# Performance work log

Measured on AMD Instinct MI355X. Metric: run time of the kernel, lower is better.

The kernel has to match this reference:

```python
import jax, jax.numpy as jnp
import numpy as np

# static multi-scale feature pyramid (strides 8/16/32/64 of ~800px input)
SPATIAL = ((100, 100), (50, 50), (25, 25), (13, 13))
L = 4          # num_levels
NH = 8         # num_heads
NP = 4         # num_points
E = 256        # embed_dim
HD = E // NH   # head dim = 32
NLAYERS = 6
FFN_DIM = 1024
T = sum(h * w for h, w in SPATIAL)  # 13294 total tokens
B = 2


def _layer_norm(x, g, b, eps=1e-5):
    m = jnp.mean(x, -1, keepdims=True)
    v = jnp.mean((x - m) ** 2, -1, keepdims=True)
    return (x - m) * jax.lax.rsqrt(v + eps) * g + b


def _get_reference_points(valid_ratios):
    # valid_ratios: [B, L, 2] (wx, hy)
    refs = []
    for lvl, (H_, W_) in enumerate(SPATIAL):
        ry, rx = jnp.meshgrid(
            jnp.linspace(0.5, H_ - 0.5, H_, dtype=jnp.float32),
            jnp.linspace(0.5, W_ - 0.5, W_, dtype=jnp.float32),
            indexing='ij')
        ry = ry.reshape(-1)[None] / (valid_ratios[:, None, lvl, 1] * H_)
        rx = rx.reshape(-1)[None] / (valid_ratios[:, None, lvl, 0] * W_)
        refs.append(jnp.stack([rx, ry], -1))            # [B, H*W, 2]
    ref = jnp.concatenate(refs, 1)                       # [B, T, 2]
    return ref[:, :, None] * valid_ratios[:, None]       # [B, T, L, 2]


def _msda(value, loc, attn_w):
    # value: [B, T, NH, HD]; loc: [B, Q, NH, L, NP, 2] in [0,1]; attn_w: [B, Q, NH, L, NP]
    Bv, Tv, H, D = value.shape
    Q = loc.shape[1]
    out = jnp.zeros((Bv, Q, H, D), value.dtype)
    start = 0
    for lvl, (h, w) in enumerate(SPATIAL):
        v = value[:, start:start + h * w].transpose(0, 2, 1, 3)  # [B, NH, hw, D]
        start += h * w
        g = loc[:, :, :, lvl]                                    # [B, Q, NH, NP, 2]
        # grid_sample semantics, align_corners=False: pixel = g*size - 0.5
        x = g[..., 0] * w - 0.5
        y = g[..., 1] * h - 0.5
        x0 = jnp.floor(x).astype(jnp.int32)
        y0 = jnp.floor(y).astype(jnp.int32)
        wx = x - x0
        wy = y - y0

        def corner(ix, iy, cw):
            valid = (ix >= 0) & (ix < w) & (iy >= 0) & (iy < h)
            idx = jnp.clip(iy, 0, h - 1) * w + jnp.clip(ix, 0, w - 1)  # [B,Q,NH,NP]
            idx_t = idx.transpose(0, 2, 1, 3).reshape(Bv, H, Q * NP)
            gath = jnp.take_along_axis(v, idx_t[..., None], axis=2)    # [B,NH,QP,D]
            gath = gath.reshape(Bv, H, Q, NP, D)
            m = valid.transpose(0, 2, 1, 3)[..., None].astype(value.dtype)
            cw_t = cw.transpose(0, 2, 1, 3)[..., None]
            return gath * m * cw_t

        samp = (corner(x0, y0, (1 - wx) * (1 - wy))
                + corner(x0 + 1, y0, wx * (1 - wy))
                + corner(x0, y0 + 1, (1 - wx) * wy)
                + corner(x0 + 1, y0 + 1, wx * wy))  # [B,NH,Q,NP,D]
        out = out + jnp.einsum('bhqpd,bqhp->bqhd', samp, attn_w[:, :, :, lvl])
    return out.reshape(Bv, Q, H * D)


# offset normalizer (W, H) per level, as in Deformable-DETR
_OFF_NORM = jnp.array([[w, h] for (h, w) in SPATIAL], jnp.float32)  # [L, 2]


def _block(src, pos, ref, mask, p):
    (Wv, bv, Woff, boff, Wattn, battn, Wout, bout,
     n1g, n1b, n2g, n2b, W1, b1, W2, b2) = p
    x = _layer_norm(src, n1g, n1b)
    q = x + pos
    value = x @ Wv + bv
    value = jnp.where(mask[:, :, None], 0.0, value).reshape(B, T, NH, HD)
    off = (q @ Woff + boff).reshape(B, T, NH, L, NP, 2)
    attn = (q @ Wattn + battn).reshape(B, T, NH, L * NP)
    attn = jax.nn.softmax(attn, -1).reshape(B, T, NH, L, NP)
    loc = ref[:, :, None, :, None, :] + off / _OFF_NORM[None, None, None, :, None, :]
    attn_out = _msda(value, loc, attn) @ Wout + bout
    src = src + attn_out
    x = _layer_norm(src, n2g, n2b)
    ffn = jax.nn.relu(x @ W1 + b1) @ W2 + b2
    return src + ffn


def setup_inputs() -> dict:
    key = jax.random.key(0)
    ks = jax.random.split(key, 24)

    def rn(k, shape, scale=0.02):
        return jax.random.normal(k, shape, jnp.float32) * scale

    inp = {
        'src': jax.random.normal(ks[0], (B, T, E), jnp.float32),
        'pos': jax.random.normal(ks[1], (B, T, E), jnp.float32),
        'valid_ratios': jnp.ones((B, L, 2), jnp.float32),
        'spatial_shapes': jnp.array(SPATIAL, jnp.int32),
        'level_start_index': jnp.array(
            np.concatenate([[0], np.cumsum([h * w for h, w in SPATIAL])[:-1]]), jnp.int32),
        'mask': jnp.zeros((B, T), bool),
        # per-layer stacked parameters [NLAYERS, ...]
        'Wv': rn(ks[2], (NLAYERS, E, E)),
        'bv': jnp.zeros((NLAYERS, E), jnp.float32),
        'Woff': rn(ks[3], (NLAYERS, E, NH * L * NP * 2)),
        'boff': rn(ks[4], (NLAYERS, NH * L * NP * 2), 0.5),
        'Wattn': rn(ks[5], (NLAYERS, E, NH * L * NP)),
        'battn': jnp.zeros((NLAYERS, NH * L * NP), jnp.float32),
        'Wout': rn(ks[6], (NLAYERS, E, E)),
        'bout': jnp.zeros((NLAYERS, E), jnp.float32),
        'n1g': jnp.ones((NLAYERS, E), jnp.float32),
        'n1b': jnp.zeros((NLAYERS, E), jnp.float32),
        'n2g': jnp.ones((NLAYERS, E), jnp.float32),
        'n2b': jnp.zeros((NLAYERS, E), jnp.float32),
        'W1': rn(ks[7], (NLAYERS, E, FFN_DIM)),
        'b1': jnp.zeros((NLAYERS, FFN_DIM), jnp.float32),
        'W2': rn(ks[8], (NLAYERS, FFN_DIM, E)),
        'b2': jnp.zeros((NLAYERS, E), jnp.float32),
    }
    return inp


def reference(src, pos, valid_ratios, spatial_shapes, level_start_index, mask,
              Wv, bv, Woff, boff, Wattn, battn, Wout, bout,
              n1g, n1b, n2g, n2b, W1, b1, W2, b2):
    # spatial_shapes / level_start_index are encoded statically in SPATIAL (values match)
    ref = _get_reference_points(valid_ratios)  # [B, T, L, 2]
    x = src
    stacked = (Wv, bv, Woff, boff, Wattn, battn, Wout, bout,
               n1g, n1b, n2g, n2b, W1, b1, W2, b2)
    for i in range(NLAYERS):
        p = tuple(a[i] for a in stacked)
        x = _block(x, pos, ref, mask, p)
    return x
```

## Files before the change

kernel.cpp:

```cpp
#include <hip/hip_runtime.h>
#include <hip/hip_bf16.h>

#define NLAYERS 6
#define Bc 2
#define Tc 13294
#define Ec 256
#define NHc 8
#define FFNc 1024

#define EPI_BIAS 0
#define EPI_MASK 1
#define EPI_RES  2
#define EPI_RELU 3
#define EPI_VALOA 4

typedef __attribute__((ext_vector_type(8))) short bf16x8;
typedef __attribute__((ext_vector_type(4))) float f32x4;

typedef __attribute__((address_space(3))) unsigned int u32_lds;
typedef __attribute__((address_space(1))) unsigned int u32_glb;

__device__ __forceinline__ void gld16(const void* g, void* l) {
    __builtin_amdgcn_global_load_lds((const u32_glb*)g, (u32_lds*)l, 16, 0, 0);
}

__device__ __forceinline__ short f2bf(float f) {
    union { float f; unsigned u; } v; v.f = f;
    unsigned r = v.u + 0x7FFFu + ((v.u >> 16) & 1u);
    return (short)(r >> 16);
}
__device__ __forceinline__ float bf2f(short s) {
    union { unsigned u; float f; } v; v.u = ((unsigned)(unsigned short)s) << 16;
    return v.f;
}
__device__ __forceinline__ float bf_lo(unsigned u) {
    union { unsigned u; float f; } v; v.u = u << 16; return v.f;
}

__global__ __launch_bounds__(256) void f2bf_kernel(
    const float* __restrict__ in, short* __restrict__ out, int n4)
{
    int i = blockIdx.x * 256 + threadIdx.x;
    if (i >= n4) return;
    float4 v = *(const float4*)(in + (size_t)i * 4);
    short4 s; s.x = f2bf(v.x); s.y = f2bf(v.y); s.z = f2bf(v.z); s.w = f2bf(v.w);
    *(short4*)(out + (size_t)i * 4) = s;
}

__global__ __launch_bounds__(256) void ln_kernel(
    const float* __restrict__ src, const float* __restrict__ pos,
    const float* __restrict__ g, const float* __restrict__ b,
    short* __restrict__ x, short* __restrict__ q, int rows)
{
    int wave = threadIdx.x >> 6;
    int lane = threadIdx.x & 63;
    int row = blockIdx.x * 4 + wave;
    if (row >= rows) return;
    const float* p = src + (size_t)row * Ec;
    float4 v = *(const float4*)(p + lane * 4);
    float s  = v.x + v.y + v.z + v.w;
    float sq = v.x*v.x + v.y*v.y + v.z*v.z + v.w*v.w;
    #pragma unroll
    for (int o = 32; o; o >>= 1) { s += __shfl_xor(s, o); sq += __shfl_xor(sq, o); }
    float mean = s * (1.f / Ec);
    float var  = sq * (1.f / Ec) - mean * mean;
    float inv  = rsqrtf(var + 1e-5f);
    float4 gg = *(const float4*)(g + lane * 4);
    float4 bb = *(const float4*)(b + lane * 4);
    float xo0 = (v.x - mean) * inv * gg.x + bb.x;
    float xo1 = (v.y - mean) * inv * gg.y + bb.y;
    float xo2 = (v.z - mean) * inv * gg.z + bb.z;
    float xo3 = (v.w - mean) * inv * gg.w + bb.w;
    short4 xs; xs.x = f2bf(xo0); xs.y = f2bf(xo1); xs.z = f2bf(xo2); xs.w = f2bf(xo3);
    *(short4*)(x + (size_t)row * Ec + lane * 4) = xs;
    float4 pp = *(const float4*)(pos + (size_t)row * Ec + lane * 4);
    short4 qs;
    qs.x = f2bf(xo0 + pp.x); qs.y = f2bf(xo1 + pp.y);
    qs.z = f2bf(xo2 + pp.z); qs.w = f2bf(xo3 + pp.w);
    *(short4*)(q + (size_t)row * Ec + lane * 4) = qs;
}

__global__ __launch_bounds__(256) void ln_bf_kernel(
    const short* __restrict__ src, const short* __restrict__ pos,
    const float* __restrict__ g, const float* __restrict__ b,
    short* __restrict__ x, short* __restrict__ q, int rows)
{
    int wave = threadIdx.x >> 6;
    int lane = threadIdx.x & 63;
    int row = blockIdx.x * 4 + wave;
    if (row >= rows) return;
    short4 v4 = *(const short4*)(src + (size_t)row * Ec + lane * 4);
    float v0 = bf2f(v4.x), v1 = bf2f(v4.y), v2 = bf2f(v4.z), v3 = bf2f(v4.w);
    float s  = v0 + v1 + v2 + v3;
    float sq = v0*v0 + v1*v1 + v2*v2 + v3*v3;
    #pragma unroll
    for (int o = 32; o; o >>= 1) { s += __shfl_xor(s, o); sq += __shfl_xor(sq, o); }
    float mean = s * (1.f / Ec);
    float var  = sq * (1.f / Ec) - mean * mean;
    float inv  = rsqrtf(var + 1e-5f);
    float4 gg = *(const float4*)(g + lane * 4);
    float4 bb = *(const float4*)(b + lane * 4);
    float xo0 = (v0 - mean) * inv * gg.x + bb.x;
    float xo1 = (v1 - mean) * inv * gg.y + bb.y;
    float xo2 = (v2 - mean) * inv * gg.z + bb.z;
    float xo3 = (v3 - mean) * inv * gg.w + bb.w;
    short4 xs; xs.x = f2bf(xo0); xs.y = f2bf(xo1); xs.z = f2bf(xo2); xs.w = f2bf(xo3);
    *(short4*)(x + (size_t)row * Ec + lane * 4) = xs;
    if (q) {
        short4 pp = *(const short4*)(pos + (size_t)row * Ec + lane * 4);
        short4 qs;
        qs.x = f2bf(xo0 + bf2f(pp.x)); qs.y = f2bf(xo1 + bf2f(pp.y));
        qs.z = f2bf(xo2 + bf2f(pp.z)); qs.w = f2bf(xo3 + bf2f(pp.w));
        *(short4*)(q + (size_t)row * Ec + lane * 4) = qs;
    }
}

__global__ __launch_bounds__(256) void transpose_all(
    const float* __restrict__ Wv,   const float* __restrict__ Woff,
    const float* __restrict__ Wattn,const float* __restrict__ Wout,
    const float* __restrict__ W1,   const float* __restrict__ W2,
    short* __restrict__ wcT, short* __restrict__ woutT,
    short* __restrict__ w1T, short* __restrict__ w2T)
{
    __shared__ float tile[32][33];
    const int l = blockIdx.z;
    const int t = blockIdx.x;
    const float* W; short* Wt; int K, N, lstr, rowOff, n0, k0;
    if (t < 64)       { W = Wv;    Wt = wcT;   K = 256;  N = 256;  lstr = 163840; rowOff = 0;
                        int u = t;        n0 = (u & 7) * 32;  k0 = (u >> 3) * 32; }
    else if (t < 128) { W = Woff;  Wt = wcT;   K = 256;  N = 256;  lstr = 163840; rowOff = 256;
                        int u = t - 64;   n0 = (u & 7) * 32;  k0 = (u >> 3) * 32; }
    else if (t < 160) { W = Wattn; Wt = wcT;   K = 256;  N = 128;  lstr = 163840; rowOff = 512;
                        int u = t - 128;  n0 = (u & 3) * 32;  k0 = (u >> 2) * 32; }
    else if (t < 224) { W = Wout;  Wt = woutT; K = 256;  N = 256;  lstr = 65536;  rowOff = 0;
                        int u = t - 160;  n0 = (u & 7) * 32;  k0 = (u >> 3) * 32; }
    else if (t < 480) { W = W1;    Wt = w1T;   K = 256;  N = 1024; lstr = 262144; rowOff = 0;
                        int u = t - 224;  n0 = (u & 31) * 32; k0 = (u >> 5) * 32; }
    else              { W = W2;    Wt = w2T;   K = 1024; N = 256;  lstr = 262144; rowOff = 0;
                        int u = t - 480;  n0 = (u & 7) * 32;  k0 = (u >> 3) * 32; }
    const float* Wl = W + (size_t)l * K * N;
    short* Wtl = Wt + (size_t)l * lstr;
    int tx = threadIdx.x & 31, ty = threadIdx.x >> 5;
    #pragma unroll
    for (int i = 0; i < 32; i += 8)
        tile[ty + i][tx] = Wl[(size_t)(k0 + ty + i) * N + n0 + tx];
    __syncthreads();
    #pragma unroll
    for (int i = 0; i < 32; i += 8)
        Wtl[(size_t)(rowOff + n0 + ty + i) * K + k0 + tx] = f2bf(tile[tx][ty + i]);
}

template<int EPI, int OBF, int RESBF>
__global__ __launch_bounds__(256) void gemm_mfma(
    const short* __restrict__ A, const short* __restrict__ A2,
    const short* __restrict__ Bt,
    const float* __restrict__ bias, const float* __restrict__ bias2,
    const float* __restrict__ bias3,
    const float* __restrict__ resf, const short* __restrict__ resb,
    const unsigned char* __restrict__ mask,
    void* __restrict__ Cout, void* __restrict__ Cout2, int M, int N, int K)
{
    __shared__ short As[2][128 * 32];
    __shared__ short Bs[2][64 * 32];
    const int tid = threadIdx.x;
    const int lane = tid & 63;
    const int wv = tid >> 6;
    const int row0 = blockIdx.x * 128;
    const int col0 = blockIdx.y * 64;
    const int mbase = (wv >> 1) * 64;
    const int nbase = (wv & 1) * 32;
    const int lr = lane & 15;
    const int kg = lane >> 4;

    const short* Ause = (EPI == EPI_VALOA && blockIdx.y >= 4) ? A2 : A;

    f32x4 zf = {0.f, 0.f, 0.f, 0.f};
    f32x4 acc[4][2];
    #pragma unroll
    for (int i = 0; i < 4; ++i)
        #pragma unroll
        for (int j = 0; j < 2; ++j) acc[i][j] = zf;

    const int scol = (lane & 3) * 8;
    const int srowA = wv * 32 + (lane >> 2);
    const short* Ap = Ause + (size_t)(row0 + srowA) * K + scol;
    const int lA0 = srowA * 32 + scol;
    const int lA1 = lA0 + 16 * 32;
    const int srowB = wv * 16 + (lane >> 2);
    const short* Bp = Bt + (size_t)(col0 + srowB) * K + scol;
    const int lB = srowB * 32 + scol;

    #define STAGE(buf, k0) do { \
        gld16(Ap + (k0),                &As[buf][lA0]); \
        gld16(Ap + (size_t)16*K + (k0), &As[buf][lA1]); \
        gld16(Bp + (k0),                &Bs[buf][lB]); \
    } while (0)

    STAGE(0, 0);
    __syncthreads();
    int cur = 0;
    for (int k0 = 0; k0 < K; k0 += 32) {
        if (k0 + 32 < K) STAGE(cur ^ 1, k0 + 32);
        bf16x8 af[4], bfr[2];
        #pragma unroll
        for (int i = 0; i < 4; ++i)
            af[i]  = *(const bf16x8*)&As[cur][(mbase + i * 16 + lr) * 32 + kg * 8];
        #pragma unroll
        for (int j = 0; j < 2; ++j)
            bfr[j] = *(const bf16x8*)&Bs[cur][(nbase + j * 16 + lr) * 32 + kg * 8];
        #pragma unroll
        for (int mi = 0; mi < 4; ++mi)
            #pragma unroll
            for (int ni = 0; ni < 2; ++ni)
                acc[mi][ni] = __builtin_amdgcn_mfma_f32_16x16x32_bf16(
                    af[mi], bfr[ni], acc[mi][ni], 0, 0, 0);
        __syncthreads();
        cur ^= 1;
    }
    #undef STAGE

    float* Cf = (float*)Cout;
    short* Cb = (short*)Cout;
    short* Vb = (short*)Cout2;
    #pragma unroll
    for (int ni = 0; ni < 2; ++ni) {
        int col = col0 + nbase + ni * 16 + lr;
        float bz;
        if (EPI == EPI_VALOA)
            bz = (col < 256) ? bias[col] : ((col < 512) ? bias2[col - 256] : bias3[col - 512]);
        else
            bz = (bias2 && col >= 256) ? bias2[col - 256] : bias[col];
        #pragma unroll
        for (int mi = 0; mi < 4; ++mi) {
            int rb = row0 + mbase + mi * 16 + kg * 4;
            #pragma unroll
            for (int j = 0; j < 4; ++j) {
                int grow = rb + j;
                if (grow >= M) continue;
                float v = acc[mi][ni][j] + bz;
                if (EPI == EPI_VALOA) {
                    if (col < 256) {
                        if (mask[grow]) v = 0.f;
                        Vb[(size_t)grow * 256 + col] = f2bf(v);
                    } else {
                        Cb[(size_t)grow * 384 + (col - 256)] = f2bf(v);
                    }
                    continue;
                }
                if (EPI == EPI_MASK) { if (mask[grow]) v = 0.f; }
                if (EPI == EPI_RES) {
                    v += RESBF ? bf2f(resb[(size_t)grow * N + col])
                               : resf[(size_t)grow * N + col];
                }
                if (EPI == EPI_RELU) v = v > 0.f ? v : 0.f;
                if (OBF) Cb[(size_t)grow * N + col] = f2bf(v);
                else     Cf[(size_t)grow * N + col] = v;
            }
        }
    }
}

__global__ __launch_bounds__(256) void msda_kernel(
    const short* __restrict__ value, const short* __restrict__ oa,
    const float* __restrict__ vr, short* __restrict__ out)
{
    __shared__ int pts[8 * 136];
    const int t = threadIdx.x;
    const int bq = blockIdx.x;
    const int b = (bq >= Tc) ? 1 : 0;
    const int qq = bq - b * Tc;

    if (t < 128) {
        const int g = t >> 4;
        const int p = t & 15;
        const int lvl = p >> 2;
        const int Wl[4] = {100, 50, 25, 13};
        const int St[4] = {0, 10000, 12500, 13125};
        float base_x, base_y;
        if (qq < 10000) {
            int qi = qq;
            base_x = (0.5f + (float)(qi % 100)) / (vr[(b*4+0)*2+0] * 100.f);
            base_y = (0.5f + (float)(qi / 100)) / (vr[(b*4+0)*2+1] * 100.f);
        } else if (qq < 12500) {
            int qi = qq - 10000;
            base_x = (0.5f + (float)(qi % 50)) / (vr[(b*4+1)*2+0] * 50.f);
            base_y = (0.5f + (float)(qi / 50)) / (vr[(b*4+1)*2+1] * 50.f);
        } else if (qq < 13125) {
            int qi = qq - 12500;
            base_x = (0.5f + (float)(qi % 25)) / (vr[(b*4+2)*2+0] * 25.f);
            base_y = (0.5f + (float)(qi / 25)) / (vr[(b*4+2)*2+1] * 25.f);
        } else {
            int qi = qq - 13125;
            base_x = (0.5f + (float)(qi % 13)) / (vr[(b*4+3)*2+0] * 13.f);
            base_y = (0.5f + (float)(qi / 13)) / (vr[(b*4+3)*2+1] * 13.f);
        }
        float logit = bf2f(oa[(size_t)bq * 384 + 256 + g * 16 + p]);
        float mx = logit;
        #pragma unroll
        for (int o = 8; o; o >>= 1) mx = fmaxf(mx, __shfl_xor(mx, o));
        float e = expf(logit - mx);
        float sum = e;
        #pragma unroll
        for (int o = 8; o; o >>= 1) sum += __shfl_xor(sum, o);
        float aw = e / sum;

        const int w = Wl[lvl], hh = Wl[lvl];
        const float refx = base_x * vr[(b*4+lvl)*2+0];
        const float refy = base_y * vr[(b*4+lvl)*2+1];
        const float ox = bf2f(oa[(size_t)bq * 384 + g * 32 + p * 2 + 0]);
        const float oy = bf2f(oa[(size_t)bq * 384 + g * 32 + p * 2 + 1]);
        float locx = refx + ox / (float)w;
        float locy = refy + oy / (float)hh;
        float xf = locx * (float)w - 0.5f;
        float yf = locy * (float)hh - 0.5f;
        float x0f = floorf(xf), y0f = floorf(yf);
        int x0 = (int)x0f, y0 = (int)y0f;
        float wx = xf - x0f, wy = yf - y0f;
        float w00 = (1.f - wx) * (1.f - wy) * aw;
        float w10 = wx * (1.f - wy) * aw;
        float w01 = (1.f - wx) * wy * aw;
        float w11 = wx * wy * aw;
        bool vx0 = (x0 >= 0) && (x0 < w);
        bool vx1 = (x0 + 1 >= 0) && (x0 + 1 < w);
        bool vy0 = (y0 >= 0) && (y0 < hh);
        bool vy1 = (y0 + 1 >= 0) && (y0 + 1 < hh);
        if (!(vx0 && vy0)) w00 = 0.f;
        if (!(vx1 && vy0)) w10 = 0.f;
        if (!(vx0 && vy1)) w01 = 0.f;
        if (!(vx1 && vy1)) w11 = 0.f;
        int cx0 = min(max(x0, 0), w - 1), cx1 = min(max(x0 + 1, 0), w - 1);
        int cy0 = min(max(y0, 0), hh - 1), cy1 = min(max(y0 + 1, 0), hh - 1);
        int rowbase = b * Tc + St[lvl];
        int slot = g * 136 + p * 8 + ((p >> 3) & 1) * 4;
        int4 wq4; wq4.x = __float_as_int(w00); wq4.y = __float_as_int(w10);
        wq4.z = __float_as_int(w01); wq4.w = __float_as_int(w11);
        int4 aq4;
        aq4.x = (rowbase + cy0 * w + cx0) * 512 + g * 64;
        aq4.y = (rowbase + cy0 * w + cx1) * 512 + g * 64;
        aq4.z = (rowbase + cy1 * w + cx0) * 512 + g * 64;
        aq4.w = (rowbase + cy1 * w + cx1) * 512 + g * 64;
        *(int4*)&pts[slot] = wq4;
        *(int4*)&pts[slot + 4] = aq4;
    }
    __syncthreads();

    const int group = t >> 5;
    const int l32 = t & 31;
    const int d4 = (l32 & 15) * 4;
    const int ph = (l32 >> 4) * 8;
    const int xw = (l32 >> 4) * 4;
    const char* vbase = (const char*)value;
    float accL = 0.f, accH = 0.f;
    #pragma unroll
    for (int j = 0; j < 8; ++j) {
        int p = ph + j;
        int slot = group * 136 + p * 8 + xw;
        int4 wq = *(const int4*)&pts[slot];
        int4 aq = *(const int4*)&pts[slot + 4];
        unsigned u0 = *(const unsigned*)(vbase + (unsigned)(aq.x + d4));
        unsigned u1 = *(const unsigned*)(vbase + (unsigned)(aq.y + d4));
        unsigned u2 = *(const unsigned*)(vbase + (unsigned)(aq.z + d4));
        unsigned u3 = *(const unsigned*)(vbase + (unsigned)(aq.w + d4));
        float w00 = __int_as_float(wq.x), w10 = __int_as_float(wq.y);
        float w01 = __int_as_float(wq.z), w11 = __int_as_float(wq.w);
        accL = fmaf(w00, bf_lo(u0), accL); accH = fmaf(w00, __int_as_float((int)u0), accH);
        accL = fmaf(w10, bf_lo(u1), accL); accH = fmaf(w10, __int_as_float((int)u1), accH);
        accL = fmaf(w01, bf_lo(u2), accL); accH = fmaf(w01, __int_as_float((int)u2), accH);
        accL = fmaf(w11, bf_lo(u3), accL); accH = fmaf(w11, __int_as_float((int)u3), accH);
    }
    accL += __shfl_xor(accL, 16);
    accH += __shfl_xor(accH, 16);
    if (l32 < 16) {
        unsigned pk = ((unsigned)(unsigned short)f2bf(accL)) |
                      (((unsigned)(unsigned short)f2bf(accH)) << 16);
        *(unsigned*)((char*)out + (size_t)bq * 512 + group * 64 + d4) = pk;
    }
}

extern "C" void kernel_launch(void* const* d_in, const int* in_sizes, int n_in,
                              void* d_out, int out_size, void* d_ws, size_t ws_size,
                              hipStream_t stream) {
    const float* src  = (const float*)d_in[0];
    const float* pos  = (const float*)d_in[1];
    const float* vr   = (const float*)d_in[2];
    const unsigned char* mask = (const unsigned char*)d_in[5];
    const float* Wv    = (const float*)d_in[6];
    const float* bv    = (const float*)d_in[7];
    const float* Woff  = (const float*)d_in[8];
    const float* boff  = (const float*)d_in[9];
    const float* Wattn = (const float*)d_in[10];
    const float* battn = (const float*)d_in[11];
    const float* Wout  = (const float*)d_in[12];
    const float* bout  = (const float*)d_in[13];
    const float* n1g   = (const float*)d_in[14];
    const float* n1b   = (const float*)d_in[15];
    const float* n2g   = (const float*)d_in[16];
    const float* n2b   = (const float*)d_in[17];
    const float* W1    = (const float*)d_in[18];
    const float* b1    = (const float*)d_in[19];
    const float* W2    = (const float*)d_in[20];
    const float* b2    = (const float*)d_in[21];
    float* out = (float*)d_out;

    const size_t R = (size_t)Bc * Tc;

    short* xb    = (short*)d_ws;
    short* qb    = xb + R * 256;
    short* valb  = qb + R * 256;
    short* msdab = valb + R * 256;
    short* oab   = msdab + R * 256;
    short* srcb  = oab + R * 384;
    short* posb  = srcb + R * 256;
    short* ln2b  = xb;
    short* hb    = qb;
    short* wcT   = posb + R * 256;
    short* woutT = wcT + 6 * 163840;
    short* w1T   = woutT + 6 * 65536;
    short* w2T   = w1T + 6 * 262144;

    transpose_all<<<dim3(736, 1, 6), 256, 0, stream>>>(
        Wv, Woff, Wattn, Wout, W1, W2, wcT, woutT, w1T, w2T);
    f2bf_kernel<<<(int)((R * 64 + 255) / 256), 256, 0, stream>>>(pos, posb, (int)(R * 64));

    const int M = (int)R;
    const int lnBlocks = (int)((R + 3) / 4);
    const int MT = (int)((R + 127) / 128);

    ln_kernel<<<lnBlocks, 256, 0, stream>>>(src, pos, n1g, n1b, xb, qb, M);

    for (int l = 0; l < NLAYERS; ++l) {
        gemm_mfma<EPI_VALOA, 1, 0><<<dim3(MT, 10), 256, 0, stream>>>(
            xb, qb, wcT + (size_t)l * 163840, bv + l * Ec, boff + l * 256, battn + l * 128,
            nullptr, nullptr, mask, oab, valb, M, 640, 256);
        msda_kernel<<<(int)R, 256, 0, stream>>>(valb, oab, vr, msdab);
        if (l == 0)
            gemm_mfma<EPI_RES, 1, 0><<<dim3(MT, 4), 256, 0, stream>>>(
                msdab, nullptr, woutT + (size_t)l * 65536, bout + l * Ec, nullptr, nullptr,
                src, nullptr, nullptr, srcb, nullptr, M, 256, 256);
        else
            gemm_mfma<EPI_RES, 1, 1><<<dim3(MT, 4), 256, 0, stream>>>(
                msdab, nullptr, woutT + (size_t)l * 65536, bout + l * Ec, nullptr, nullptr,
                nullptr, srcb, nullptr, srcb, nullptr, M, 256, 256);
        ln_bf_kernel<<<lnBlocks, 256, 0, stream>>>(srcb, nullptr, n2g + l * Ec, n2b + l * Ec,
                                                   ln2b, nullptr, M);
        gemm_mfma<EPI_RELU, 1, 0><<<dim3(MT, 16), 256, 0, stream>>>(
            ln2b, nullptr, w1T + (size_t)l * 262144, b1 + l * FFNc, nullptr, nullptr,
            nullptr, nullptr, nullptr, hb, nullptr, M, 1024, 256);
        if (l < NLAYERS - 1) {
            gemm_mfma<EPI_RES, 1, 1><<<dim3(MT, 4), 256, 0, stream>>>(
                hb, nullptr, w2T + (size_t)l * 262144, b2 + l * Ec, nullptr, nullptr,
                nullptr, srcb, nullptr, srcb, nullptr, M, 256, 1024);
            ln_bf_kernel<<<lnBlocks, 256, 0, stream>>>(srcb, posb, n1g + (l + 1) * Ec,
                                                       n1b + (l + 1) * Ec, xb, qb, M);
        } else {
            gemm_mfma<EPI_RES, 0, 1><<<dim3(MT, 4), 256, 0, stream>>>(
                hb, nullptr, w2T + (size_t)l * 262144, b2 + l * Ec, nullptr, nullptr,
                nullptr, srcb, nullptr, out, nullptr, M, 256, 1024);
        }
    }
}
```

Before: 1.138 ms.

## Drop bf16 pos pre-conversion and simplify MSDA sampling-location math

Removes the separate f2bf kernel that converted pos to bf16; the layer-norm kernel now reads fp32 pos directly. This saves one launch and a full pass over pos, but the five later LN calls each read twice as many pos bytes. The MSDA kernel also folds the reference-point and offset arithmetic so the per-level divide and multiply cancel, and replaces expf with __expf. The new location math can round slightly differently from the old path.

```diff
diff --git a/kernel.cpp b/kernel.cpp
--- a/kernel.cpp
+++ b/kernel.cpp
@@ -35,16 +35,6 @@
 }
 __device__ __forceinline__ float bf_lo(unsigned u) {
     union { unsigned u; float f; } v; v.u = u << 16; return v.f;
-}
-
-__global__ __launch_bounds__(256) void f2bf_kernel(
-    const float* __restrict__ in, short* __restrict__ out, int n4)
-{
-    int i = blockIdx.x * 256 + threadIdx.x;
-    if (i >= n4) return;
-    float4 v = *(const float4*)(in + (size_t)i * 4);
-    short4 s; s.x = f2bf(v.x); s.y = f2bf(v.y); s.z = f2bf(v.z); s.w = f2bf(v.w);
-    *(short4*)(out + (size_t)i * 4) = s;
 }
 
 __global__ __launch_bounds__(256) void ln_kernel(
@@ -81,7 +71,7 @@
 }
 
 __global__ __launch_bounds__(256) void ln_bf_kernel(
-    const short* __restrict__ src, const short* __restrict__ pos,
+    const short* __restrict__ src, const float* __restrict__ pos,
     const float* __restrict__ g, const float* __restrict__ b,
     short* __restrict__ x, short* __restrict__ q, int rows)
 {
@@ -107,10 +97,10 @@
     short4 xs; xs.x = f2bf(xo0); xs.y = f2bf(xo1); xs.z = f2bf(xo2); xs.w = f2bf(xo3);
     *(short4*)(x + (size_t)row * Ec + lane * 4) = xs;
     if (q) {
-        short4 pp = *(const short4*)(pos + (size_t)row * Ec + lane * 4);
+        float4 pp = *(const float4*)(pos + (size_t)row * Ec + lane * 4);
         short4 qs;
-        qs.x = f2bf(xo0 + bf2f(pp.x)); qs.y = f2bf(xo1 + bf2f(pp.y));
-        qs.z = f2bf(xo2 + bf2f(pp.z)); qs.w = f2bf(xo3 + bf2f(pp.w));
+        qs.x = f2bf(xo0 + pp.x); qs.y = f2bf(xo1 + pp.y);
+        qs.z = f2bf(xo2 + pp.z); qs.w = f2bf(xo3 + pp.w);
         *(short4*)(q + (size_t)row * Ec + lane * 4) = qs;
     }
 }
@@ -274,45 +264,34 @@
         const int g = t >> 4;
         const int p = t & 15;
         const int lvl = p >> 2;
-        const int Wl[4] = {100, 50, 25, 13};
         const int St[4] = {0, 10000, 12500, 13125};
-        float base_x, base_y;
-        if (qq < 10000) {
-            int qi = qq;
-            base_x = (0.5f + (float)(qi % 100)) / (vr[(b*4+0)*2+0] * 100.f);
-            base_y = (0.5f + (float)(qi / 100)) / (vr[(b*4+0)*2+1] * 100.f);
-        } else if (qq < 12500) {
-            int qi = qq - 10000;
-            base_x = (0.5f + (float)(qi % 50)) / (vr[(b*4+1)*2+0] * 50.f);
-            base_y = (0.5f + (float)(qi / 50)) / (vr[(b*4+1)*2+1] * 50.f);
-        } else if (qq < 13125) {
-            int qi = qq - 12500;
-            base_x = (0.5f + (float)(qi % 25)) / (vr[(b*4+2)*2+0] * 25.f);
-            base_y = (0.5f + (float)(qi / 25)) / (vr[(b*4+2)*2+1] * 25.f);
-        } else {
-            int qi = qq - 13125;
-            base_x = (0.5f + (float)(qi % 13)) / (vr[(b*4+3)*2+0] * 13.f);
-            base_y = (0.5f + (float)(qi / 13)) / (vr[(b*4+3)*2+1] * 13.f);
-        }
+        int qi, Wq, qlvl;
+        if (qq < 10000)      { qlvl = 0; qi = qq;         Wq = 100; }
+        else if (qq < 12500) { qlvl = 1; qi = qq - 10000; Wq = 50; }
+        else if (qq < 13125) { qlvl = 2; qi = qq - 12500; Wq = 25; }
+        else                 { qlvl = 3; qi = qq - 13125; Wq = 13; }
+        float base_x = (0.5f + (float)(qi % Wq)) / (vr[(b*4+qlvl)*2+0] * (float)Wq);
+        float base_y = (0.5f + (float)(qi / Wq)) / (vr[(b*4+qlvl)*2+1] * (float)Wq);
+
         float logit = bf2f(oa[(size_t)bq * 384 + 256 + g * 16 + p]);
         float mx = logit;
         #pragma unroll
         for (int o = 8; o; o >>= 1) mx = fmaxf(mx, __shfl_xor(mx, o));
-        float e = expf(logit - mx);
+        float e = __expf(logit - mx);
         float sum = e;
         #pragma unroll
         for (int o = 8; o; o >>= 1) sum += __shfl_xor(sum, o);
         float aw = e / sum;
 
-        const int w = Wl[lvl], hh = Wl[lvl];
-        const float refx = base_x * vr[(b*4+lvl)*2+0];
-        const float refy = base_y * vr[(b*4+lvl)*2+1];
+        const int w = (lvl == 0) ? 100 : ((lvl == 1) ? 50 : ((lvl == 2) ? 25 : 13));
+        const int hh = w;
+        const float wf = (float)w;
+        const float refxw = base_x * vr[(b*4+lvl)*2+0] * wf;
+        const float refyw = base_y * vr[(b*4+lvl)*2+1] * wf;
         const float ox = bf2f(oa[(size_t)bq * 384 + g * 32 + p * 2 + 0]);
         const float oy = bf2f(oa[(size_t)bq * 384 + g * 32 + p * 2 + 1]);
-        float locx = refx + ox / (float)w;
-        float locy = refy + oy / (float)hh;
-        float xf = locx * (float)w - 0.5f;
-        float yf = locy * (float)hh - 0.5f;
+        float xf = refxw + ox - 0.5f;
+        float yf = refyw + oy - 0.5f;
         float x0f = floorf(xf), y0f = floorf(yf);
         int x0 = (int)x0f, y0 = (int)y0f;
         float wx = xf - x0f, wy = yf - y0f;
@@ -410,17 +389,15 @@
     short* msdab = valb + R * 256;
     short* oab   = msdab + R * 256;
     short* srcb  = oab + R * 384;
-    short* posb  = srcb + R * 256;
     short* ln2b  = xb;
     short* hb    = qb;
-    short* wcT   = posb + R * 256;
+    short* wcT   = srcb + R * 256;
     short* woutT = wcT + 6 * 163840;
     short* w1T   = woutT + 6 * 65536;
     short* w2T   = w1T + 6 * 262144;
 
     transpose_all<<<dim3(736, 1, 6), 256, 0, stream>>>(
         Wv, Woff, Wattn, Wout, W1, W2, wcT, woutT, w1T, w2T);
-    f2bf_kernel<<<(int)((R * 64 + 255) / 256), 256, 0, stream>>>(pos, posb, (int)(R * 64));
 
     const int M = (int)R;
     const int lnBlocks = (int)((R + 3) / 4);
@@ -450,7 +427,7 @@
             gemm_mfma<EPI_RES, 1, 1><<<dim3(MT, 4), 256, 0, stream>>>(
                 hb, nullptr, w2T + (size_t)l * 262144, b2 + l * Ec, nullptr, nullptr,
                 nullptr, srcb, nullptr, srcb, nullptr, M, 256, 1024);
-            ln_bf_kernel<<<lnBlocks, 256, 0, stream>>>(srcb, posb, n1g + (l + 1) * Ec,
+            ln_bf_kernel<<<lnBlocks, 256, 0, stream>>>(srcb, pos, n1g + (l + 1) * Ec,
                                                        n1b + (l + 1) * Ec, xb, qb, M);
         } else {
             gemm_mfma<EPI_RES, 0, 1><<<dim3(MT, 4), 256, 0, stream>>>(
```

Result: no change. 1.132 ms (-0.5%).
